# Performance work log

Hardware: AMD Instinct MI355X
Metric: run time of the kernel (lower is better)

Reference implementation:

```python
import jax, jax.numpy as jnp
import numpy as np

N, E, D, L = 100000, 500000, 128, 5
NUM_ATOM_FEATS, ATOM_VOCAB = 9, 120
NUM_BOND_FEATS, BOND_VOCAB = 3, 8
BN_EPS = 1e-5


def setup_inputs() -> dict:
    key = jax.random.key(0)
    ks = jax.random.split(key, 16)
    inp = {
        "x": jax.random.randint(ks[0], (N, NUM_ATOM_FEATS), 0, ATOM_VOCAB),
        "edge_index": jax.random.randint(ks[1], (2, E), 0, N),
        "edge_attr": jax.random.randint(ks[2], (E, NUM_BOND_FEATS), 0, BOND_VOCAB),
        "edge_weight": jax.random.uniform(ks[3], (E,), dtype=jnp.float32),
        # parameters
        "atom_emb": jax.random.normal(ks[4], (NUM_ATOM_FEATS, ATOM_VOCAB, D), dtype=jnp.float32) * 0.02,
        "bond_emb": jax.random.normal(ks[5], (L, NUM_BOND_FEATS, BOND_VOCAB, D), dtype=jnp.float32) * 0.02,
        "eps": jnp.zeros((L,), dtype=jnp.float32),
        "W1": jax.random.normal(ks[6], (L, D, 2 * D), dtype=jnp.float32) / np.sqrt(D),
        "b1": jnp.zeros((L, 2 * D), dtype=jnp.float32),
        "g1": jnp.ones((L, 2 * D), dtype=jnp.float32),
        "bt1": jnp.zeros((L, 2 * D), dtype=jnp.float32),
        "W2": jax.random.normal(ks[7], (L, 2 * D, D), dtype=jnp.float32) / np.sqrt(2 * D),
        "b2": jnp.zeros((L, D), dtype=jnp.float32),
        "g_out": jnp.ones((L, D), dtype=jnp.float32),
        "bt_out": jnp.zeros((L, D), dtype=jnp.float32),
    }
    return inp


def _batchnorm(h, g, b):
    # training-mode BN over node axis, biased variance (matches torch BN normalization)
    mu = jnp.mean(h, axis=0)
    var = jnp.mean((h - mu) ** 2, axis=0)
    return g * (h - mu) * jax.lax.rsqrt(var + BN_EPS) + b


def reference(x, edge_index, edge_attr, edge_weight,
              atom_emb, bond_emb, eps, W1, b1, g1, bt1, W2, b2, g_out, bt_out):
    # AtomEncoder: sum per-column embedding lookups -> [N, D]
    h = atom_emb[jnp.arange(NUM_ATOM_FEATS)[None, :], x].sum(axis=1)
    src, dst = edge_index[0], edge_index[1]
    ew = edge_weight[:, None]
    for l in range(L):
        # BondEncoder for layer l -> [E, D]
        e = bond_emb[l][jnp.arange(NUM_BOND_FEATS)[None, :], edge_attr].sum(axis=1)
        # message: relu(x_j + edge_emb) * edge_weight ; aggregate: scatter-add at dst
        m = jax.nn.relu(h[src] + e) * ew
        agg = jax.ops.segment_sum(m, dst, num_segments=N)
        z = (1.0 + eps[l]) * h + agg
        # GIN MLP: Linear -> BN -> ReLU -> Linear
        z = jax.nn.relu(_batchnorm(z @ W1[l] + b1[l], g1[l], bt1[l])) @ W2[l] + b2[l]
        # outer BatchNorm; dropout is identity in eval mode
        h_new = _batchnorm(z, g_out[l], bt_out[l])
        h = h_new if l == L - 1 else jax.nn.relu(h_new)
    return h
```

## Files before the change

kernel.cpp:

```cpp
#include <hip/hip_runtime.h>
#include <hip/hip_bf16.h>
#include <hip/hip_fp16.h>

#define NN 100000
#define EE 500000
#define NP 100096

typedef _Float16 f16;
typedef __attribute__((ext_vector_type(8))) _Float16 f16x8;
typedef __attribute__((ext_vector_type(4))) _Float16 f16x4;
typedef __attribute__((ext_vector_type(4))) float f32x4;

__global__ __launch_bounds__(256) void prep_kernel(const float* __restrict__ W1,
                                                   const float* __restrict__ W2,
                                                   const float* __restrict__ bemb,
                                                   f16* __restrict__ w1f,
                                                   f16* __restrict__ w2f,
                                                   f16* __restrict__ bembf) {
  int gid = blockIdx.x * 256 + threadIdx.x;
  if (gid < 163840) {
    int l = gid / 32768; int rem = gid % 32768;
    int k = rem / 256;   int n = rem % 256;
    int ctg = n >> 4, m = n & 15;
    int c = k >> 5, q = (k >> 3) & 3, e = k & 7;
    int lane = q * 16 + m;
    w1f[l * 32768 + ((ctg * 4 + c) * 64 + lane) * 8 + e] = (f16)W1[gid];
  } else if (gid < 327680) {
    int g = gid - 163840;
    int l = g / 32768; int rem = g % 32768;
    int k = rem / 128; int n = rem % 128;
    int ctg = n >> 4, m = n & 15;
    int c = k >> 5, q = (k >> 3) & 3, e = k & 7;
    int lane = q * 16 + m;
    w2f[l * 32768 + ((ctg * 8 + c) * 64 + lane) * 8 + e] = (f16)W2[g];
  } else if (gid < 343040) {
    int g = gid - 327680;
    bembf[g] = (f16)bemb[g];
  }
}

__global__ __launch_bounds__(256) void zero_deg_kernel(int* __restrict__ deg) {
  int i = blockIdx.x * 256 + threadIdx.x;
  if (i < NN) deg[i] = 0;
}

__global__ __launch_bounds__(256) void hist_kernel(const int* __restrict__ ei, int* __restrict__ deg) {
  int e = blockIdx.x * 256 + threadIdx.x;
  if (e < EE) atomicAdd(&deg[ei[EE + e]], 1);
}

__global__ __launch_bounds__(256) void scan1_kernel(const int* __restrict__ deg,
                                                    int* __restrict__ offs,
                                                    int* __restrict__ bsum) {
  __shared__ int sh[256];
  int b = blockIdx.x, t = threadIdx.x;
  int base = b * 1024 + t * 4;
  int v[4];
  int s = 0;
#pragma unroll
  for (int i = 0; i < 4; ++i) { v[i] = (base + i < NN) ? deg[base + i] : 0; s += v[i]; }
  sh[t] = s;
  __syncthreads();
  for (int off = 1; off < 256; off <<= 1) {
    int x = (t >= off) ? sh[t - off] : 0;
    __syncthreads();
    sh[t] += x;
    __syncthreads();
  }
  int excl = sh[t] - s;
  if (t == 255) bsum[b] = sh[255];
  int run = excl;
#pragma unroll
  for (int i = 0; i < 4; ++i) {
    if (base + i < NN) offs[base + i] = run;
    run += v[i];
  }
}

__global__ void scan2_kernel(int* __restrict__ bsum, int nb) {
  if (threadIdx.x == 0 && blockIdx.x == 0) {
    int run = 0;
    for (int i = 0; i < nb; ++i) { int v = bsum[i]; bsum[i] = run; run += v; }
  }
}

__global__ __launch_bounds__(256) void scan3_kernel(int* __restrict__ offs,
                                                    const int* __restrict__ bsum,
                                                    int* __restrict__ cursor) {
  int i = blockIdx.x * 256 + threadIdx.x;
  if (i < NN) {
    int v = offs[i] + bsum[i >> 10];
    offs[i] = v;
    cursor[i] = v;
  } else if (i == NN) {
    offs[NN] = EE;
  }
}

__global__ __launch_bounds__(256) void scatter_kernel(const int* __restrict__ ei,
                                                      const int* __restrict__ ea,
                                                      const float* __restrict__ ew,
                                                      int* __restrict__ cursor,
                                                      int* __restrict__ pk,
                                                      float* __restrict__ wsrt) {
  int e = blockIdx.x * 256 + threadIdx.x;
  if (e >= EE) return;
  int dst = ei[EE + e];
  int pos = atomicAdd(&cursor[dst], 1);
  int src = ei[e];
  int a0 = ea[e * 3 + 0], a1 = ea[e * 3 + 1], a2 = ea[e * 3 + 2];
  pk[pos] = src | (a0 << 17) | (a1 << 20) | (a2 << 23);
  wsrt[pos] = ew[e];
}

__global__ __launch_bounds__(256) void zero_slices_kernel(float* __restrict__ p) {
  int i = blockIdx.x * 256 + threadIdx.x;
  *(float4*)(p + i * 4) = float4{0.f, 0.f, 0.f, 0.f};
}

__global__ __launch_bounds__(256) void atom_kernel(const int* __restrict__ x,
                                                   const float* __restrict__ aemb,
                                                   f16* __restrict__ hf) {
  int gid = blockIdx.x * 256 + threadIdx.x;
  int n = gid >> 5, qq = gid & 31;
  if (n >= NN) return;
  float4 s = {0.f, 0.f, 0.f, 0.f};
#pragma unroll
  for (int f = 0; f < 9; ++f) {
    int xi = x[n * 9 + f];
    float4 v = *(const float4*)(aemb + (f * 120 + xi) * 128 + qq * 4);
    s.x += v.x; s.y += v.y; s.z += v.z; s.w += v.w;
  }
  f16x4 o;
  o[0] = (f16)s.x; o[1] = (f16)s.y; o[2] = (f16)s.z; o[3] = (f16)s.w;
  *(f16x4*)(hf + (long)n * 128 + qq * 4) = o;
}

__global__ __launch_bounds__(256) void edge_agg_kernel(const int* __restrict__ offs,
                                                       const int* __restrict__ pk,
                                                       const float* __restrict__ wsrt,
                                                       const f16* __restrict__ bembf,
                                                       const float* __restrict__ eps,
                                                       const f16* __restrict__ hf,
                                                       f16* __restrict__ zb) {
  int gid = blockIdx.x * 256 + threadIdx.x;
  int n = gid >> 4, d0 = (gid & 15) * 8;
  if (n >= NN) {
    f16x8 z = {0, 0, 0, 0, 0, 0, 0, 0};
    *(f16x8*)(zb + (long)n * 128 + d0) = z;
    return;
  }
  int s0 = offs[n], s1 = offs[n + 1];
  float e1 = 1.f + eps[0];
  f16x8 hn = *(const f16x8*)(hf + (long)n * 128 + d0);
  float acc[8];
#pragma unroll
  for (int i = 0; i < 8; ++i) acc[i] = e1 * (float)hn[i];
  for (int e = s0; e < s1; ++e) {
    int p = pk[e];
    float w = wsrt[e];
    int src = p & 131071;
    f16x8 b0 = *(const f16x8*)(bembf + (((p >> 17) & 7)) * 128 + d0);
    f16x8 b1 = *(const f16x8*)(bembf + (8 + ((p >> 20) & 7)) * 128 + d0);
    f16x8 b2 = *(const f16x8*)(bembf + (16 + ((p >> 23) & 7)) * 128 + d0);
    f16x8 hs = *(const f16x8*)(hf + (long)src * 128 + d0);
    f16x8 sm = hs + b0 + b1 + b2;
#pragma unroll
    for (int i = 0; i < 8; ++i) {
      float sv = (float)sm[i];
      acc[i] += fmaxf(sv, 0.f) * w;
    }
  }
  f16x8 o;
#pragma unroll
  for (int i = 0; i < 8; ++i) o[i] = (f16)acc[i];
  *(f16x8*)(zb + (long)n * 128 + d0) = o;
}

__global__ __launch_bounds__(256) void edge_agg_bn_kernel(const int* __restrict__ offs,
                                                          const int* __restrict__ pk,
                                                          const float* __restrict__ wsrt,
                                                          const f16* __restrict__ bembf,
                                                          const float* __restrict__ eps, int l,
                                                          const f16* __restrict__ t2,
                                                          const float* __restrict__ sum2s,
                                                          const float* __restrict__ sq2s,
                                                          const float* __restrict__ g2,
                                                          const float* __restrict__ bt2,
                                                          float* __restrict__ s1z,
                                                          f16* __restrict__ zb) {
  __shared__ float sc2[128], sh2[128];
  const int tid = threadIdx.x;
  if (tid < 128) {
    float s = 0.f, s2 = 0.f;
#pragma unroll
    for (int k = 0; k < 16; ++k) { s += sum2s[k * 128 + tid]; s2 += sq2s[k * 128 + tid]; }
    float mu = s * (1.f / NN);
    float var = fmaxf(s2 * (1.f / NN) - mu * mu, 0.f);
    float is = rsqrtf(var + 1e-5f);
    float sc = g2[tid] * is;
    sc2[tid] = sc;
    sh2[tid] = bt2[tid] - mu * sc;
  }
  if (blockIdx.x == 0) {
#pragma unroll
    for (int j = 0; j < 8; ++j)
      *(float4*)(s1z + (j * 256 + tid) * 4) = float4{0.f, 0.f, 0.f, 0.f};
  }
  __syncthreads();
  int gid = blockIdx.x * 256 + tid;
  int n = gid >> 4, d0 = (gid & 15) * 8;
  if (n >= NN) {
    f16x8 z = {0, 0, 0, 0, 0, 0, 0, 0};
    *(f16x8*)(zb + (long)n * 128 + d0) = z;
    return;
  }
  float4 svA = *(const float4*)(sc2 + d0), svB = *(const float4*)(sc2 + d0 + 4);
  float4 shA = *(const float4*)(sh2 + d0), shB = *(const float4*)(sh2 + d0 + 4);
  float sv[8] = {svA.x, svA.y, svA.z, svA.w, svB.x, svB.y, svB.z, svB.w};
  float hv[8] = {shA.x, shA.y, shA.z, shA.w, shB.x, shB.y, shB.z, shB.w};
  int s0 = offs[n], s1 = offs[n + 1];
  float e1 = 1.f + eps[l];
  f16x8 hn = *(const f16x8*)(t2 + (long)n * 128 + d0);
  float acc[8];
#pragma unroll
  for (int i = 0; i < 8; ++i)
    acc[i] = e1 * fmaxf((float)hn[i] * sv[i] + hv[i], 0.f);
  for (int e = s0; e < s1; ++e) {
    int p = pk[e];
    float w = wsrt[e];
    int src = p & 131071;
    f16x8 b0 = *(const f16x8*)(bembf + (((p >> 17) & 7)) * 128 + d0);
    f16x8 b1 = *(const f16x8*)(bembf + (8 + ((p >> 20) & 7)) * 128 + d0);
    f16x8 b2 = *(const f16x8*)(bembf + (16 + ((p >> 23) & 7)) * 128 + d0);
    f16x8 hs = *(const f16x8*)(t2 + (long)src * 128 + d0);
    f16x8 bs = b0 + b1 + b2;
#pragma unroll
    for (int i = 0; i < 8; ++i) {
      float y = fmaxf((float)hs[i] * sv[i] + hv[i], 0.f);
      float s = y + (float)bs[i];
      acc[i] += fmaxf(s, 0.f) * w;
    }
  }
  f16x8 o;
#pragma unroll
  for (int i = 0; i < 8; ++i) o[i] = (f16)acc[i];
  *(f16x8*)(zb + (long)n * 128 + d0) = o;
}

__global__ __launch_bounds__(256) void gemm1_kernel(const f16* __restrict__ zb,
                                                    const f16* __restrict__ w1f,
                                                    f16* __restrict__ t1f,
                                                    float* __restrict__ sum1s,
                                                    float* __restrict__ sq1s,
                                                    float* __restrict__ s2z) {
  __shared__ __align__(16) char ldsraw[17408];
  const int tid = threadIdx.x;
  const int lane = tid & 63, w = tid >> 6;
  const int wr = w >> 1, wc = w & 1;
  const int m = lane & 15, q = lane >> 4;
  const int rbase = blockIdx.x * 64;
  const int cb = blockIdx.y;
  const int slice = blockIdx.x & 15;

  if (blockIdx.x == 0 && cb == 0) {
#pragma unroll
    for (int j = 0; j < 4; ++j)
      *(float4*)(s2z + (j * 256 + tid) * 4) = float4{0.f, 0.f, 0.f, 0.f};
  }

  f16x8 B[4][4];
#pragma unroll
  for (int ct = 0; ct < 4; ++ct)
#pragma unroll
    for (int c = 0; c < 4; ++c)
      B[ct][c] = *(const f16x8*)(w1f + (((cb * 8 + wc * 4 + ct) * 4 + c) * 64 + lane) * 8);

  {
    f16x8 st[4];
    const int tofs = tid * 16;
#pragma unroll
    for (int j = 0; j < 4; ++j)
      st[j] = *(const f16x8*)(zb + (long)rbase * 128 + (tofs + j * 4096) / 2);
#pragma unroll
    for (int j = 0; j < 4; ++j) {
      int ofs = tofs + j * 4096;
      int row = ofs >> 8, colb = ofs & 255;
      *(f16x8*)(ldsraw + row * 256 + (colb ^ ((row & 7) << 4))) = st[j];
    }
  }
  __syncthreads();

  f16x8 A[2][4];
#pragma unroll
  for (int rt = 0; rt < 2; ++rt) {
    int row = wr * 32 + rt * 16 + m;
    int rs = row * 256, sw = (row & 7) << 4;
#pragma unroll
    for (int c = 0; c < 4; ++c) {
      int colb = c * 64 + q * 16;
      A[rt][c] = *(const f16x8*)(ldsraw + rs + (colb ^ sw));
    }
  }

  f32x4 acc[2][4];
  const f32x4 zf = {0.f, 0.f, 0.f, 0.f};
#pragma unroll
  for (int a = 0; a < 2; ++a)
#pragma unroll
    for (int b = 0; b < 4; ++b) acc[a][b] = zf;

#pragma unroll
  for (int c = 0; c < 4; ++c)
#pragma unroll
    for (int rt = 0; rt < 2; ++rt)
#pragma unroll
      for (int ct = 0; ct < 4; ++ct)
        acc[rt][ct] = __builtin_amdgcn_mfma_f32_16x16x32_f16(A[rt][c], B[ct][c], acc[rt][ct], 0, 0, 0);

  __syncthreads();
  f16 (*sh)[136] = (f16(*)[136])ldsraw;

#pragma unroll
  for (int ct = 0; ct < 4; ++ct) {
    int lc = wc * 64 + ct * 16 + m;
    int gc = cb * 128 + lc;
    float s = 0.f, s2 = 0.f;
#pragma unroll
    for (int rt = 0; rt < 2; ++rt) {
      int lr = wr * 32 + rt * 16 + q * 4;
#pragma unroll
      for (int i = 0; i < 4; ++i) {
        float v = acc[rt][ct][i];
        s += v; s2 += v * v;
        sh[lr + i][lc] = (f16)v;
      }
    }
    s  += __shfl_xor(s, 16);  s  += __shfl_xor(s, 32);
    s2 += __shfl_xor(s2, 16); s2 += __shfl_xor(s2, 32);
    if (q == 0) {
      unsafeAtomicAdd(&sum1s[slice * 256 + gc], s);
      unsafeAtomicAdd(&sq1s[slice * 256 + gc], s2);
    }
  }
  __syncthreads();
  const int colc = tid & 15, r0 = tid >> 4;
#pragma unroll
  for (int j = 0; j < 4; ++j) {
    int r = j * 16 + r0;
    f16x8 v = *(const f16x8*)(&sh[r][colc * 8]);
    *(f16x8*)(t1f + (long)(rbase + r) * 256 + cb * 128 + colc * 8) = v;
  }
}

__global__ __launch_bounds__(256) void gemm2_kernel(const f16* __restrict__ a1,
                                                    const f16* __restrict__ w2f,
                                                    const float* __restrict__ sum1s,
                                                    const float* __restrict__ sq1s,
                                                    const float* __restrict__ g1,
                                                    const float* __restrict__ bt1,
                                                    f16* __restrict__ t2out,
                                                    float* __restrict__ sum2s,
                                                    float* __restrict__ sq2s) {
  __shared__ __align__(16) char ldsraw[34816];
  float* sc1 = (float*)(ldsraw + 32768);
  float* sh1 = (float*)(ldsraw + 33792);
  const int tid = threadIdx.x;
  const int lane = tid & 63, w = tid >> 6;
  const int wr = w >> 1, wc = w & 1;
  const int m = lane & 15, q = lane >> 4;
  const int rbase = blockIdx.x * 64;
  const int slice = blockIdx.x & 15;

  f16x8 st[8];
  const int tofs = tid * 16;
#pragma unroll
  for (int j = 0; j < 8; ++j)
    st[j] = *(const f16x8*)(a1 + (long)rbase * 256 + (tofs + j * 4096) / 2);

  {
    float s = 0.f, s2 = 0.f;
#pragma unroll
    for (int k = 0; k < 16; ++k) { s += sum1s[k * 256 + tid]; s2 += sq1s[k * 256 + tid]; }
    float mu = s * (1.f / NN);
    float var = fmaxf(s2 * (1.f / NN) - mu * mu, 0.f);
    float is = rsqrtf(var + 1e-5f);
    float sc = g1[tid] * is;
    sc1[tid] = sc;
    sh1[tid] = bt1[tid] - mu * sc;
  }
  __syncthreads();

  {
    const int k0 = (tid & 31) * 8;
    float4 sa = *(const float4*)(sc1 + k0);
    float4 sb = *(const float4*)(sc1 + k0 + 4);
    float4 ha = *(const float4*)(sh1 + k0);
    float4 hb = *(const float4*)(sh1 + k0 + 4);
#pragma unroll
    for (int j = 0; j < 8; ++j) {
      int ofs = tofs + j * 4096;
      int row = ofs >> 9, colb = ofs & 511;
      f16x8 u = st[j], o;
      o[0] = (f16)fmaxf((float)u[0] * sa.x + ha.x, 0.f);
      o[1] = (f16)fmaxf((float)u[1] * sa.y + ha.y, 0.f);
      o[2] = (f16)fmaxf((float)u[2] * sa.z + ha.z, 0.f);
      o[3] = (f16)fmaxf((float)u[3] * sa.w + ha.w, 0.f);
      o[4] = (f16)fmaxf((float)u[4] * sb.x + hb.x, 0.f);
      o[5] = (f16)fmaxf((float)u[5] * sb.y + hb.y, 0.f);
      o[6] = (f16)fmaxf((float)u[6] * sb.z + hb.z, 0.f);
      o[7] = (f16)fmaxf((float)u[7] * sb.w + hb.w, 0.f);
      *(f16x8*)(ldsraw + row * 512 + (colb ^ ((row & 7) << 4))) = o;
    }
  }
  __syncthreads();

  f32x4 acc[2][4];
  const f32x4 zf = {0.f, 0.f, 0.f, 0.f};
#pragma unroll
  for (int a = 0; a < 2; ++a)
#pragma unroll
    for (int b = 0; b < 4; ++b) acc[a][b] = zf;

#pragma unroll
  for (int hh = 0; hh < 2; ++hh) {
    f16x8 A[2][4], B[4][4];
#pragma unroll
    for (int rt = 0; rt < 2; ++rt) {
      int row = wr * 32 + rt * 16 + m;
      int rs = row * 512, sw = (row & 7) << 4;
#pragma unroll
      for (int c = 0; c < 4; ++c) {
        int colb = (hh * 4 + c) * 64 + q * 16;
        A[rt][c] = *(const f16x8*)(ldsraw + rs + (colb ^ sw));
      }
    }
#pragma unroll
    for (int ct = 0; ct < 4; ++ct)
#pragma unroll
      for (int c = 0; c < 4; ++c)
        B[ct][c] = *(const f16x8*)(w2f + (((wc * 4 + ct) * 8 + hh * 4 + c) * 64 + lane) * 8);
#pragma unroll
    for (int c = 0; c < 4; ++c)
#pragma unroll
      for (int rt = 0; rt < 2; ++rt)
#pragma unroll
        for (int ct = 0; ct < 4; ++ct)
          acc[rt][ct] = __builtin_amdgcn_mfma_f32_16x16x32_f16(A[rt][c], B[ct][c], acc[rt][ct], 0, 0, 0);
  }

  __syncthreads();
  f16 (*sh)[136] = (f16(*)[136])ldsraw;

#pragma unroll
  for (int ct = 0; ct < 4; ++ct) {
    int gc = wc * 64 + ct * 16 + m;
    float s = 0.f, s2 = 0.f;
#pragma unroll
    for (int rt = 0; rt < 2; ++rt) {
      int grow = rbase + wr * 32 + rt * 16 + q * 4;
      int lr = wr * 32 + rt * 16 + q * 4;
#pragma unroll
      for (int i = 0; i < 4; ++i) {
        float v = acc[rt][ct][i];
        float vv = (grow + i < NN) ? v : 0.f;
        s += vv; s2 += vv * vv;
        sh[lr + i][gc] = (f16)v;
      }
    }
    s  += __shfl_xor(s, 16);  s  += __shfl_xor(s, 32);
    s2 += __shfl_xor(s2, 16); s2 += __shfl_xor(s2, 32);
    if (q == 0) {
      unsafeAtomicAdd(&sum2s[slice * 128 + gc], s);
      unsafeAtomicAdd(&sq2s[slice * 128 + gc], s2);
    }
  }
  __syncthreads();
  const int colc = tid & 15, r0 = tid >> 4;
#pragma unroll
  for (int j = 0; j < 4; ++j) {
    int r = j * 16 + r0;
    f16x8 v = *(const f16x8*)(&sh[r][colc * 8]);
    *(f16x8*)(t2out + (long)(rbase + r) * 128 + colc * 8) = v;
  }
}

__global__ __launch_bounds__(256) void apply_kernel(const f16* __restrict__ t2,
                                                    const float* __restrict__ sum2s,
                                                    const float* __restrict__ sq2s,
                                                    const float* __restrict__ g2,
                                                    const float* __restrict__ bt2,
                                                    float* __restrict__ outp) {
  __shared__ float sc2[128], sh2[128];
  const int tid = threadIdx.x;
  if (tid < 128) {
    float s = 0.f, s2 = 0.f;
#pragma unroll
    for (int k = 0; k < 16; ++k) { s += sum2s[k * 128 + tid]; s2 += sq2s[k * 128 + tid]; }
    float mu = s * (1.f / NN);
    float var = fmaxf(s2 * (1.f / NN) - mu * mu, 0.f);
    float is = rsqrtf(var + 1e-5f);
    float sc = g2[tid] * is;
    sc2[tid] = sc;
    sh2[tid] = bt2[tid] - mu * sc;
  }
  __syncthreads();
  const int rbase = blockIdx.x * 64;
#pragma unroll
  for (int k = 0; k < 4; ++k) {
    int ci = tid + k * 256;
    int r = ci >> 4, c8 = ci & 15;
    int row = rbase + r;
    if (row >= NN) continue;
    f16x8 u = *(const f16x8*)(t2 + (long)row * 128 + c8 * 8);
    float4 sa = *(const float4*)(sc2 + c8 * 8);
    float4 sb = *(const float4*)(sc2 + c8 * 8 + 4);
    float4 ha = *(const float4*)(sh2 + c8 * 8);
    float4 hb = *(const float4*)(sh2 + c8 * 8 + 4);
    float4 o0 = {(float)u[0] * sa.x + ha.x, (float)u[1] * sa.y + ha.y,
                 (float)u[2] * sa.z + ha.z, (float)u[3] * sa.w + ha.w};
    float4 o1 = {(float)u[4] * sb.x + hb.x, (float)u[5] * sb.y + hb.y,
                 (float)u[6] * sb.z + hb.z, (float)u[7] * sb.w + hb.w};
    *(float4*)(outp + (long)row * 128 + c8 * 8) = o0;
    *(float4*)(outp + (long)row * 128 + c8 * 8 + 4) = o1;
  }
}

extern "C" void kernel_launch(void* const* d_in, const int* in_sizes, int n_in,
                              void* d_out, int out_size, void* d_ws, size_t ws_size,
                              hipStream_t stream) {
  (void)in_sizes; (void)n_in; (void)out_size; (void)ws_size;
  const int*   x      = (const int*)d_in[0];
  const int*   ei     = (const int*)d_in[1];
  const int*   ea     = (const int*)d_in[2];
  const float* ew     = (const float*)d_in[3];
  const float* aemb   = (const float*)d_in[4];
  const float* bemb   = (const float*)d_in[5];
  const float* eps    = (const float*)d_in[6];
  const float* W1     = (const float*)d_in[7];
  const float* g1     = (const float*)d_in[9];
  const float* bt1    = (const float*)d_in[10];
  const float* W2     = (const float*)d_in[11];
  const float* g_out  = (const float*)d_in[13];
  const float* bt_out = (const float*)d_in[14];

  float* outp = (float*)d_out;

  char* ws = (char*)d_ws;
  f16*   hf    = (f16*)(ws);
  f16*   zb    = (f16*)(ws + 25624576);
  f16*   t1f   = (f16*)(ws + 51249152);
  f16*   w1f   = (f16*)(ws + 102498304);
  f16*   w2f   = (f16*)(ws + 102825984);
  f16*   bembf = (f16*)(ws + 103153664);
  float* slices= (float*)(ws + 103187456);
  int*   deg    = (int*)(ws + 103236608);
  int*   offs   = (int*)(ws + 103636608);
  int*   cursor = (int*)(ws + 104036624);
  int*   bsum   = (int*)(ws + 104436624);
  int*   pk     = (int*)(ws + 104437024);
  float* wsrt   = (float*)(ws + 106437024);

  float* sum1s = slices;
  float* sq1s  = slices + 4096;
  float* sum2s = slices + 8192;
  float* sq2s  = slices + 10240;

  prep_kernel<<<1340, 256, 0, stream>>>(W1, W2, bemb, w1f, w2f, bembf);
  zero_deg_kernel<<<391, 256, 0, stream>>>(deg);
  hist_kernel<<<1954, 256, 0, stream>>>(ei, deg);
  scan1_kernel<<<98, 256, 0, stream>>>(deg, offs, bsum);
  scan2_kernel<<<1, 64, 0, stream>>>(bsum, 98);
  scan3_kernel<<<392, 256, 0, stream>>>(offs, bsum, cursor);
  scatter_kernel<<<1954, 256, 0, stream>>>(ei, ea, ew, cursor, pk, wsrt);
  zero_slices_kernel<<<12, 256, 0, stream>>>(slices);
  atom_kernel<<<12500, 256, 0, stream>>>(x, aemb, hf);

  for (int l = 0; l < 5; ++l) {
    if (l == 0) {
      edge_agg_kernel<<<6256, 256, 0, stream>>>(offs, pk, wsrt, bembf, eps, hf, zb);
    } else {
      edge_agg_bn_kernel<<<6256, 256, 0, stream>>>(offs, pk, wsrt, bembf + l * 3072, eps, l,
                                                   hf, sum2s, sq2s,
                                                   g_out + (l - 1) * 128, bt_out + (l - 1) * 128,
                                                   sum1s, zb);
    }
    gemm1_kernel<<<dim3(1564, 2), 256, 0, stream>>>(zb, w1f + l * 32768, t1f, sum1s, sq1s, sum2s);
    gemm2_kernel<<<1564, 256, 0, stream>>>(t1f, w2f + l * 32768, sum1s, sq1s,
                                           g1 + l * 256, bt1 + l * 256, hf, sum2s, sq2s);
    if (l == 4)
      apply_kernel<<<1564, 256, 0, stream>>>(hf, sum2s, sq2s, g_out + 512, bt_out + 512, outp);
  }
}
```

Baseline: 626.8 us.

## Precompute combined bond embedding table and pipeline edge gathers

Builds a per-layer table of all 512 combined bond-embedding sums so each edge reads one row instead of three and adds them. The edge aggregation loops now prefetch the next edge's index, weight and gathered rows before computing the current one. The BN-apply and ReLU in the gather path move to packed f16 arithmetic, and the gemm1 grid is transposed so blocks sharing rows run together. The table reuses workspace that held the degree and cursor arrays, and f16 BN math slightly reduces precision.

```diff
diff --git a/kernel.cpp b/kernel.cpp
--- a/kernel.cpp
+++ b/kernel.cpp
@@ -11,12 +11,22 @@
 typedef __attribute__((ext_vector_type(4))) _Float16 f16x4;
 typedef __attribute__((ext_vector_type(4))) float f32x4;
 
+static __device__ __forceinline__ f16x8 relu8(f16x8 a) {
+#if __has_builtin(__builtin_elementwise_max)
+  f16x8 z = {0, 0, 0, 0, 0, 0, 0, 0};
+  return __builtin_elementwise_max(a, z);
+#else
+  f16x8 r;
+#pragma unroll
+  for (int i = 0; i < 8; ++i) r[i] = (a[i] > (f16)0) ? a[i] : (f16)0;
+  return r;
+#endif
+}
+
 __global__ __launch_bounds__(256) void prep_kernel(const float* __restrict__ W1,
                                                    const float* __restrict__ W2,
-                                                   const float* __restrict__ bemb,
                                                    f16* __restrict__ w1f,
-                                                   f16* __restrict__ w2f,
-                                                   f16* __restrict__ bembf) {
+                                                   f16* __restrict__ w2f) {
   int gid = blockIdx.x * 256 + threadIdx.x;
   if (gid < 163840) {
     int l = gid / 32768; int rem = gid % 32768;
@@ -33,10 +43,19 @@
     int c = k >> 5, q = (k >> 3) & 3, e = k & 7;
     int lane = q * 16 + m;
     w2f[l * 32768 + ((ctg * 8 + c) * 64 + lane) * 8 + e] = (f16)W2[g];
-  } else if (gid < 343040) {
-    int g = gid - 327680;
-    bembf[g] = (f16)bemb[g];
-  }
+  }
+}
+
+__global__ __launch_bounds__(256) void bondtab_kernel(const float* __restrict__ bemb,
+                                                      f16* __restrict__ tab) {
+  int gid = blockIdx.x * 256 + threadIdx.x;
+  int l = gid >> 16;
+  int rem = gid & 65535;
+  int combo = rem >> 7, d = rem & 127;
+  int a0 = combo & 7, a1 = (combo >> 3) & 7, a2 = combo >> 6;
+  const float* bl = bemb + l * 3072;
+  float v = bl[a0 * 128 + d] + bl[1024 + a1 * 128 + d] + bl[2048 + a2 * 128 + d];
+  tab[gid] = (f16)v;
 }
 
 __global__ __launch_bounds__(256) void zero_deg_kernel(int* __restrict__ deg) {
@@ -139,7 +158,7 @@
 __global__ __launch_bounds__(256) void edge_agg_kernel(const int* __restrict__ offs,
                                                        const int* __restrict__ pk,
                                                        const float* __restrict__ wsrt,
-                                                       const f16* __restrict__ bembf,
+                                                       const f16* __restrict__ tab,
                                                        const float* __restrict__ eps,
                                                        const f16* __restrict__ hf,
                                                        f16* __restrict__ zb) {
@@ -156,20 +175,27 @@
   float acc[8];
 #pragma unroll
   for (int i = 0; i < 8; ++i) acc[i] = e1 * (float)hn[i];
-  for (int e = s0; e < s1; ++e) {
-    int p = pk[e];
-    float w = wsrt[e];
-    int src = p & 131071;
-    f16x8 b0 = *(const f16x8*)(bembf + (((p >> 17) & 7)) * 128 + d0);
-    f16x8 b1 = *(const f16x8*)(bembf + (8 + ((p >> 20) & 7)) * 128 + d0);
-    f16x8 b2 = *(const f16x8*)(bembf + (16 + ((p >> 23) & 7)) * 128 + d0);
-    f16x8 hs = *(const f16x8*)(hf + (long)src * 128 + d0);
-    f16x8 sm = hs + b0 + b1 + b2;
-#pragma unroll
-    for (int i = 0; i < 8; ++i) {
-      float sv = (float)sm[i];
-      acc[i] += fmaxf(sv, 0.f) * w;
-    }
+
+  int e = s0;
+  int pc; float wc; f16x8 hc, bc;
+  if (e < s1) {
+    pc = pk[e]; wc = wsrt[e];
+    hc = *(const f16x8*)(hf + (long)(pc & 131071) * 128 + d0);
+    bc = *(const f16x8*)(tab + ((pc >> 17) & 511) * 128 + d0);
+  }
+  for (; e < s1; ++e) {
+    int en = e + 1;
+    bool more = en < s1;
+    int pn; float wn; f16x8 hx, bx;
+    if (more) {
+      pn = pk[en]; wn = wsrt[en];
+      hx = *(const f16x8*)(hf + (long)(pn & 131071) * 128 + d0);
+      bx = *(const f16x8*)(tab + ((pn >> 17) & 511) * 128 + d0);
+    }
+    f16x8 sm = relu8(hc + bc);
+#pragma unroll
+    for (int i = 0; i < 8; ++i) acc[i] += (float)sm[i] * wc;
+    if (more) { pc = pn; wc = wn; hc = hx; bc = bx; }
   }
   f16x8 o;
 #pragma unroll
@@ -180,7 +206,7 @@
 __global__ __launch_bounds__(256) void edge_agg_bn_kernel(const int* __restrict__ offs,
                                                           const int* __restrict__ pk,
                                                           const float* __restrict__ wsrt,
-                                                          const f16* __restrict__ bembf,
+                                                          const f16* __restrict__ tab,
                                                           const float* __restrict__ eps, int l,
                                                           const f16* __restrict__ t2,
                                                           const float* __restrict__ sum2s,
@@ -219,6 +245,10 @@
   float4 shA = *(const float4*)(sh2 + d0), shB = *(const float4*)(sh2 + d0 + 4);
   float sv[8] = {svA.x, svA.y, svA.z, svA.w, svB.x, svB.y, svB.z, svB.w};
   float hv[8] = {shA.x, shA.y, shA.z, shA.w, shB.x, shB.y, shB.z, shB.w};
+  f16x8 sv8, hv8;
+#pragma unroll
+  for (int i = 0; i < 8; ++i) { sv8[i] = (f16)sv[i]; hv8[i] = (f16)hv[i]; }
+
   int s0 = offs[n], s1 = offs[n + 1];
   float e1 = 1.f + eps[l];
   f16x8 hn = *(const f16x8*)(t2 + (long)n * 128 + d0);
@@ -226,21 +256,28 @@
 #pragma unroll
   for (int i = 0; i < 8; ++i)
     acc[i] = e1 * fmaxf((float)hn[i] * sv[i] + hv[i], 0.f);
-  for (int e = s0; e < s1; ++e) {
-    int p = pk[e];
-    float w = wsrt[e];
-    int src = p & 131071;
-    f16x8 b0 = *(const f16x8*)(bembf + (((p >> 17) & 7)) * 128 + d0);
-    f16x8 b1 = *(const f16x8*)(bembf + (8 + ((p >> 20) & 7)) * 128 + d0);
-    f16x8 b2 = *(const f16x8*)(bembf + (16 + ((p >> 23) & 7)) * 128 + d0);
-    f16x8 hs = *(const f16x8*)(t2 + (long)src * 128 + d0);
-    f16x8 bs = b0 + b1 + b2;
-#pragma unroll
-    for (int i = 0; i < 8; ++i) {
-      float y = fmaxf((float)hs[i] * sv[i] + hv[i], 0.f);
-      float s = y + (float)bs[i];
-      acc[i] += fmaxf(s, 0.f) * w;
-    }
+
+  int e = s0;
+  int pc; float wc; f16x8 hc, bc;
+  if (e < s1) {
+    pc = pk[e]; wc = wsrt[e];
+    hc = *(const f16x8*)(t2 + (long)(pc & 131071) * 128 + d0);
+    bc = *(const f16x8*)(tab + ((pc >> 17) & 511) * 128 + d0);
+  }
+  for (; e < s1; ++e) {
+    int en = e + 1;
+    bool more = en < s1;
+    int pn; float wn; f16x8 hx, bx;
+    if (more) {
+      pn = pk[en]; wn = wsrt[en];
+      hx = *(const f16x8*)(t2 + (long)(pn & 131071) * 128 + d0);
+      bx = *(const f16x8*)(tab + ((pn >> 17) & 511) * 128 + d0);
+    }
+    f16x8 y = relu8(hc * sv8 + hv8);
+    f16x8 sm = relu8(y + bc);
+#pragma unroll
+    for (int i = 0; i < 8; ++i) acc[i] += (float)sm[i] * wc;
+    if (more) { pc = pn; wc = wn; hc = hx; bc = bx; }
   }
   f16x8 o;
 #pragma unroll
@@ -259,11 +296,11 @@
   const int lane = tid & 63, w = tid >> 6;
   const int wr = w >> 1, wc = w & 1;
   const int m = lane & 15, q = lane >> 4;
-  const int rbase = blockIdx.x * 64;
-  const int cb = blockIdx.y;
-  const int slice = blockIdx.x & 15;
-
-  if (blockIdx.x == 0 && cb == 0) {
+  const int cb = blockIdx.x;
+  const int rbase = blockIdx.y * 64;
+  const int slice = blockIdx.y & 15;
+
+  if (blockIdx.y == 0 && cb == 0) {
 #pragma unroll
     for (int j = 0; j < 4; ++j)
       *(float4*)(s2z + (j * 256 + tid) * 4) = float4{0.f, 0.f, 0.f, 0.f};
@@ -552,40 +589,41 @@
   f16*   t1f   = (f16*)(ws + 51249152);
   f16*   w1f   = (f16*)(ws + 102498304);
   f16*   w2f   = (f16*)(ws + 102825984);
-  f16*   bembf = (f16*)(ws + 103153664);
-  float* slices= (float*)(ws + 103187456);
-  int*   deg    = (int*)(ws + 103236608);
-  int*   offs   = (int*)(ws + 103636608);
-  int*   cursor = (int*)(ws + 104036624);
-  int*   bsum   = (int*)(ws + 104436624);
-  int*   pk     = (int*)(ws + 104437024);
-  float* wsrt   = (float*)(ws + 106437024);
+  float* slices= (float*)(ws + 103153664);
+  int*   offs  = (int*)(ws + 103202816);
+  int*   bsum  = (int*)(ws + 103602848);
+  int*   deg   = (int*)(ws + 103603360);
+  int*   cursor= (int*)(ws + 104003360);
+  f16*   bsumtab = (f16*)(ws + 103603360);
+  int*   pk    = (int*)(ws + 104403360);
+  float* wsrt  = (float*)(ws + 106403360);
 
   float* sum1s = slices;
   float* sq1s  = slices + 4096;
   float* sum2s = slices + 8192;
   float* sq2s  = slices + 10240;
 
-  prep_kernel<<<1340, 256, 0, stream>>>(W1, W2, bemb, w1f, w2f, bembf);
+  prep_kernel<<<1280, 256, 0, stream>>>(W1, W2, w1f, w2f);
   zero_deg_kernel<<<391, 256, 0, stream>>>(deg);
   hist_kernel<<<1954, 256, 0, stream>>>(ei, deg);
   scan1_kernel<<<98, 256, 0, stream>>>(deg, offs, bsum);
   scan2_kernel<<<1, 64, 0, stream>>>(bsum, 98);
   scan3_kernel<<<392, 256, 0, stream>>>(offs, bsum, cursor);
   scatter_kernel<<<1954, 256, 0, stream>>>(ei, ea, ew, cursor, pk, wsrt);
+  bondtab_kernel<<<1280, 256, 0, stream>>>(bemb, bsumtab);
   zero_slices_kernel<<<12, 256, 0, stream>>>(slices);
   atom_kernel<<<12500, 256, 0, stream>>>(x, aemb, hf);
 
   for (int l = 0; l < 5; ++l) {
     if (l == 0) {
-      edge_agg_kernel<<<6256, 256, 0, stream>>>(offs, pk, wsrt, bembf, eps, hf, zb);
+      edge_agg_kernel<<<6256, 256, 0, stream>>>(offs, pk, wsrt, bsumtab, eps, hf, zb);
     } else {
-      edge_agg_bn_kernel<<<6256, 256, 0, stream>>>(offs, pk, wsrt, bembf + l * 3072, eps, l,
+      edge_agg_bn_kernel<<<6256, 256, 0, stream>>>(offs, pk, wsrt, bsumtab + l * 65536, eps, l,
                                                    hf, sum2s, sq2s,
                                                    g_out + (l - 1) * 128, bt_out + (l - 1) * 128,
                                                    sum1s, zb);
     }
-    gemm1_kernel<<<dim3(1564, 2), 256, 0, stream>>>(zb, w1f + l * 32768, t1f, sum1s, sq1s, sum2s);
+    gemm1_kernel<<<dim3(2, 1564), 256, 0, stream>>>(zb, w1f + l * 32768, t1f, sum1s, sq1s, sum2s);
     gemm2_kernel<<<1564, 256, 0, stream>>>(t1f, w2f + l * 32768, sum1s, sq1s,
                                            g1 + l * 256, bt1 + l * 256, hf, sum2s, sq2s);
     if (l == 4)
```

Result: faster. 598.4 us (-4.5%).
